# Kernel optimization log

Measured on AMD Instinct MI355X. Metric: run time of the kernel, lower is better.

The kernel has to match this reference:

```python
import jax, jax.numpy as jnp
import numpy as np

CODE_LEN = 1024
INFO_LEN = 512
BATCH = 2048
ITERS = 5
CLIP = 15.0
N_STAGES = 10  # log2(CODE_LEN)
DESIGN_SNR = 0.0


def _bhattacharyya_info_idx(N, K, snr_db):
    # standard polar code construction: Bhattacharyya parameter recursion
    z = np.array([np.exp(-10.0 ** (snr_db / 10.0))], dtype=np.float64)
    while z.size < N:
        z = np.concatenate([2.0 * z - z ** 2, z ** 2])
    return np.sort(np.argsort(z)[:K]).astype(np.int32)


def setup_inputs() -> dict:
    key = jax.random.key(0)
    rx = jax.random.normal(key, (BATCH, CODE_LEN), dtype=jnp.float32) * 4.0  # channel LLRs
    info_idx = jnp.asarray(_bhattacharyya_info_idx(CODE_LEN, INFO_LEN, DESIGN_SNR))
    return {"rx": rx, "info_idx": info_idx}


def _split(x, s):
    # pair elements (i, i + 2^s) within blocks of size 2^(s+1)
    B, N = x.shape
    st = 1 << s
    xr = x.reshape(B, N // (2 * st), 2, st)
    return xr[:, :, 0, :], xr[:, :, 1, :]


def _merge(u, l, s):
    B = u.shape[0]
    return jnp.stack([u, l], axis=2).reshape(B, -1)


def _f(a, b):
    # min-sum check-node update
    return jnp.sign(a) * jnp.sign(b) * jnp.minimum(jnp.abs(a), jnp.abs(b))


def _clip(x):
    return jnp.clip(x, -CLIP, CLIP)


def _iterate_right(right, left):
    # sweep info side (stage 0) -> channel side (stage n)
    cur = right[:, 0]
    stages = [cur]
    for s in range(N_STAGES):
        r_u, r_l = _split(cur, s)
        l_u, l_l = _split(left[:, s + 1], s)
        n_u = _clip(_f(r_u, l_l + r_l))
        n_l = _clip(_f(r_u, l_u) + r_l)
        cur = _merge(n_u, n_l, s)
        stages.append(cur)
    return jnp.stack(stages, axis=1)


def _iterate_left(right, left):
    # sweep channel side (stage n) -> info side (stage 0)
    cur = left[:, N_STAGES]
    stages = [cur]
    for s in range(N_STAGES - 1, -1, -1):
        l_u, l_l = _split(cur, s)
        r_u, r_l = _split(right[:, s], s)
        n_u = _clip(_f(l_u, l_l + r_l))
        n_l = _clip(_f(r_u, l_u) + l_l)
        cur = _merge(n_u, n_l, s)
        stages.append(cur)
    return jnp.stack(stages[::-1], axis=1)


def reference(rx, info_idx):
    B = rx.shape[0]
    mask = jnp.zeros((CODE_LEN,), rx.dtype).at[info_idx].set(1.0)
    # frozen positions carry +clip LLR, info positions 0 (crc=[], so total_info_bits == info mask)
    right = jnp.zeros((B, N_STAGES + 1, CODE_LEN), rx.dtype).at[:, 0].set((1.0 - mask) * CLIP)
    left = jnp.zeros_like(right).at[:, N_STAGES].set(rx)
    u_list = []
    for _ in range(ITERS):  # filter_in_iterations_eval=False -> all rows active every iteration
        right = _iterate_right(right, left)
        left = _iterate_left(right, left)
        u = left[:, 0] + right[:, 0]
        u_list.append(jnp.take(u, info_idx, axis=1))
    u_list.append(u_list[-1])  # u_list[-1] scatter reduces to last iterate when all rows active
    return jnp.stack(u_list)  # [ITERS+1, B, INFO_LEN]
```

## Files before the change

kernel.cpp:

```cpp
#include <hip/hip_runtime.h>

constexpr int CODE_LEN = 1024;
constexpr int INFO_LEN = 512;
constexpr int BATCH    = 2048;
constexpr int ITERS    = 5;
#define CLIPV 15.0f

__device__ __forceinline__ float fop(float a, float b) {
    unsigned x; float m, r;
    asm("v_xor_b32 %0, %1, %2" : "=v"(x) : "v"(a), "v"(b));
    asm("v_min_f32 %0, |%1|, |%2|" : "=v"(m) : "v"(a), "v"(b));
    asm("v_and_or_b32 %0, %1, %2, %3" : "=v"(r) : "v"(x), "s"(0x80000000u), "v"(m));
    return r;
}
__device__ __forceinline__ float clipf(float x) {
    return __builtin_amdgcn_fmed3f(x, -CLIPV, CLIPV);
}


#define RSTEP0(A, B) do { \
    float bu0=(B)[0], bl0=(B)[1], bu1=(B)[2], bl1=(B)[3]; \
    (B)[0]=fop((A)[0], bl0+(A)[1]); \
    (B)[1]=clipf(fop((A)[0], bu0)+(A)[1]); \
    (B)[2]=fop((A)[2], bl1+(A)[3]); \
    (B)[3]=clipf(fop((A)[2], bu1)+(A)[3]); } while(0)
#define RSTEP1(A, B) do { \
    float bu0=(B)[0], bl0=(B)[2], bu1=(B)[1], bl1=(B)[3]; \
    (B)[0]=fop((A)[0], bl0+(A)[2]); \
    (B)[2]=clipf(fop((A)[0], bu0)+(A)[2]); \
    (B)[1]=fop((A)[1], bl1+(A)[3]); \
    (B)[3]=clipf(fop((A)[1], bu1)+(A)[3]); } while(0)
#define LSTEP0(A, B) do { \
    float au0=(A)[0], al0=(A)[1], au1=(A)[2], al1=(A)[3]; \
    (A)[0]=fop((B)[0], (B)[1]+al0); \
    (A)[1]=clipf(fop(au0, (B)[0])+(B)[1]); \
    (A)[2]=fop((B)[2], (B)[3]+al1); \
    (A)[3]=clipf(fop(au1, (B)[2])+(B)[3]); } while(0)
#define LSTEP1(A, B) do { \
    float au0=(A)[0], al0=(A)[2], au1=(A)[1], al1=(A)[3]; \
    (A)[0]=fop((B)[0], (B)[2]+al0); \
    (A)[2]=clipf(fop(au0, (B)[0])+(B)[2]); \
    (A)[1]=fop((B)[1], (B)[3]+al1); \
    (A)[3]=clipf(fop(au1, (B)[1])+(B)[3]); } while(0)
#define LSTEP1C(A, B) do { \
    float au0=(A)[0], al0=(A)[2], au1=(A)[1], al1=(A)[3]; \
    (A)[0]=clipf(fop((B)[0], (B)[2]+al0)); \
    (A)[2]=clipf(fop(au0, (B)[0])+(B)[2]); \
    (A)[1]=clipf(fop((B)[1], (B)[3]+al1)); \
    (A)[3]=clipf(fop(au1, (B)[1])+(B)[3]); } while(0)
#define RSTEP0Z(A, B) do { \
    (B)[0]=fop((A)[0], (A)[1]); (B)[1]=(A)[1]; \
    (B)[2]=fop((A)[2], (A)[3]); (B)[3]=(A)[3]; } while(0)
#define RSTEP1Z(A, B) do { \
    (B)[0]=fop((A)[0], (A)[2]); (B)[2]=(A)[2]; \
    (B)[1]=fop((A)[1], (A)[3]); (B)[3]=(A)[3]; } while(0)

#define XBAR() do { \
    asm volatile("s_waitcnt lgkmcnt(0)" ::: "memory"); \
    __builtin_amdgcn_s_barrier(); \
    __builtin_amdgcn_sched_barrier(0); } while(0)

#define CONV_W(arr, WBASE, RBASE) do { \
    *(float4*)&WB[WBASE] = make_float4((arr)[0], (arr)[1], (arr)[2], (arr)[3]); \
    const float* rp_ = &WB[RBASE]; \
    float c0_ = rp_[0], c1_ = rp_[64], c2_ = rp_[128], c3_ = rp_[192]; \
    (arr)[0]=c0_; (arr)[1]=c1_; (arr)[2]=c2_; (arr)[3]=c3_; } while(0)

#define CONV_X(arr, XBUF) do { \
    float T0_ = mb0 ? (arr)[1] : (arr)[0]; \
    float T1_ = mb0 ? (arr)[0] : (arr)[1]; \
    float T2_ = mb0 ? (arr)[3] : (arr)[2]; \
    float T3_ = mb0 ? (arr)[2] : (arr)[3]; \
    float U0_ = mb1 ? T2_ : T0_; \
    float U1_ = mb1 ? T3_ : T1_; \
    float U2_ = mb1 ? T0_ : T2_; \
    float U3_ = mb1 ? T1_ : T3_; \
    *(float4*)&(XBUF)[wX] = make_float4(U0_, U1_, U2_, U3_); \
    XBAR(); \
    const float* xp_ = &(XBUF)[rX]; \
    float c0_ = xp_[0], c1_ = xp_[256], c2_ = xp_[512], c3_ = xp_[768]; \
    (arr)[0]=c0_; (arr)[1]=c1_; (arr)[2]=c2_; (arr)[3]=c3_; } while(0)

__global__ __launch_bounds__(256, 4) void polar_bp_r10(const float* __restrict__ rx,
                                                       const int* __restrict__ info,
                                                       float* __restrict__ out) {
    __shared__ int   RK[CODE_LEN];
    __shared__ float WB[CODE_LEN];
    __shared__ float XB0[CODE_LEN];
    __shared__ float XB1[CODE_LEN];

    const int t = threadIdx.x;
    const int b = blockIdx.x;

    *(int4*)&RK[t * 4] = make_int4(-1, -1, -1, -1);
    __syncthreads();
#pragma unroll
    for (int k = 0; k < 2; ++k) {
        int kk = t + 256 * k;
        int p  = info[kk];
        int fl = (p & 3) | (((p >> 6) & 3) << 2) | (((p >> 4) & 3) << 4)
               | (((p >> 2) & 3) << 6) | (((p >> 8) & 3) << 8);
        RK[fl] = kk;
    }
    __syncthreads();

    const int l6 = t & 63;
    const int w  = t >> 6;
    const int wbase = w * 256;
    const int wW4 = wbase + 4 * l6;
    const int rW4 = wbase + 4 * (l6 & 15) + ((l6 >> 4) & 3);
    const int wW2 = wbase + 4 * ((l6 & 3) | (((l6 >> 4) & 3) << 2) | (((l6 >> 2) & 3) << 4));
    const int rW2 = wbase + 4 * ((l6 & 3) | (((l6 >> 4) & 3) << 2)) + ((l6 >> 2) & 3);
    const int wW0 = wbase + 4 * (((l6 >> 2) & 15) | ((l6 & 3) << 4));
    const int rW0 = wbase + 4 * ((l6 >> 2) & 15) + (l6 & 3);
    const int  mX  = (l6 >> 3) & 3;
    const bool mb0 = (l6 & 8)  != 0;
    const bool mb1 = (l6 & 16) != 0;
    const int  wX  = 4 * l6 + 256 * w;
    const int  rX  = 4 * l6 + (w ^ mX);

    const int4 rkv = *(const int4*)&RK[t * 4];
    float fr[4];
    fr[0] = rkv.x < 0 ? CLIPV : 0.f;  fr[1] = rkv.y < 0 ? CLIPV : 0.f;
    fr[2] = rkv.z < 0 ? CLIPV : 0.f;  fr[3] = rkv.w < 0 ? CLIPV : 0.f;

    float S[10][4];
    {
        const float* rxb = rx + (size_t)b * CODE_LEN
                         + ((t >> 6) & 3) * 64 + (t & 3) * 16
                         + ((t >> 2) & 3) * 4 + ((t >> 4) & 3);
        S[9][0] = rxb[0];   S[9][1] = rxb[256];
        S[9][2] = rxb[512]; S[9][3] = rxb[768];
    }

    RSTEP0Z(fr, S[0]);
    RSTEP1Z(S[0], S[1]);
    CONV_W(S[1], wW4, rW4);
    RSTEP0Z(S[1], S[2]);
    RSTEP1Z(S[2], S[3]);
    CONV_W(S[3], wW2, rW2);
    RSTEP0Z(S[3], S[4]);
    RSTEP1Z(S[4], S[5]);
    CONV_W(S[5], wW0, rW0);
    RSTEP0Z(S[5], S[6]);
    RSTEP1Z(S[6], S[7]);
    CONV_X(S[7], XB0);
    RSTEP0Z(S[7], S[8]);

    float v0, v1, v2, v3;
    float* ob = out + (size_t)b * INFO_LEN;
    const size_t obstride = (size_t)BATCH * INFO_LEN;

#pragma unroll 1
    for (int it = 0; it < ITERS; ++it) {
        LSTEP1C(S[8], S[9]);
        LSTEP0(S[7], S[8]);
        CONV_X(S[7], XB1);
        LSTEP1(S[6], S[7]);
        LSTEP0(S[5], S[6]);
        CONV_W(S[5], wW0, rW0);
        LSTEP1(S[4], S[5]);
        LSTEP0(S[3], S[4]);
        CONV_W(S[3], wW2, rW2);
        LSTEP1(S[2], S[3]);
        LSTEP0(S[1], S[2]);
        CONV_W(S[1], wW4, rW4);
        LSTEP1(S[0], S[1]);
        v0 = fop(S[0][0], S[0][1] + fr[1]);
        v1 = clipf(fop(fr[0], S[0][0]) + S[0][1]);
        v2 = fop(S[0][2], S[0][3] + fr[3]);
        v3 = clipf(fop(fr[2], S[0][2]) + S[0][3]);
        if (rkv.x >= 0) ob[rkv.x] = v0;
        if (rkv.y >= 0) ob[rkv.y] = v1;
        if (rkv.z >= 0) ob[rkv.z] = v2;
        if (rkv.w >= 0) ob[rkv.w] = v3;
        ob += obstride;
        if (it != ITERS - 1) {
            RSTEP0(fr, S[0]);
            RSTEP1(S[0], S[1]);
            CONV_W(S[1], wW4, rW4);
            RSTEP0(S[1], S[2]);
            RSTEP1(S[2], S[3]);
            CONV_W(S[3], wW2, rW2);
            RSTEP0(S[3], S[4]);
            RSTEP1(S[4], S[5]);
            CONV_W(S[5], wW0, rW0);
            RSTEP0(S[5], S[6]);
            RSTEP1(S[6], S[7]);
            CONV_X(S[7], XB0);
            RSTEP0(S[7], S[8]);
        }
    }
    if (rkv.x >= 0) ob[rkv.x] = v0;
    if (rkv.y >= 0) ob[rkv.y] = v1;
    if (rkv.z >= 0) ob[rkv.z] = v2;
    if (rkv.w >= 0) ob[rkv.w] = v3;
}

extern "C" void kernel_launch(void* const* d_in, const int* in_sizes, int n_in,
                              void* d_out, int out_size, void* d_ws, size_t ws_size,
                              hipStream_t stream) {
    const float* rx   = (const float*)d_in[0];
    const int*   info = (const int*)d_in[1];
    float*       outp = (float*)d_out;
    polar_bp_r10<<<dim3(BATCH), dim3(256), 0, stream>>>(rx, info, outp);
}
```

Baseline: 32.71 us.

## Decode two codewords per block to amortize barriers and raise ILP

Each block now processes two batch rows, interleaving their stage updates so the two independent dependency chains can overlap. The cross-wave exchanges for both rows share a single barrier, and the grid is halved. This targets barrier and latency stalls per codeword. In exchange it doubles register state per thread (launch bounds lowered to 2 blocks per SM), uses more shared memory, and gives fewer blocks, all of which may reduce occupancy.

```diff
diff --git a/kernel.cpp b/kernel.cpp
--- a/kernel.cpp
+++ b/kernel.cpp
@@ -60,13 +60,13 @@
     __builtin_amdgcn_s_barrier(); \
     __builtin_amdgcn_sched_barrier(0); } while(0)
 
-#define CONV_W(arr, WBASE, RBASE) do { \
-    *(float4*)&WB[WBASE] = make_float4((arr)[0], (arr)[1], (arr)[2], (arr)[3]); \
-    const float* rp_ = &WB[RBASE]; \
+#define CONV_W(arr, WBp, WB_, RB_) do { \
+    *(float4*)&(WBp)[WB_] = make_float4((arr)[0], (arr)[1], (arr)[2], (arr)[3]); \
+    const float* rp_ = &(WBp)[RB_]; \
     float c0_ = rp_[0], c1_ = rp_[64], c2_ = rp_[128], c3_ = rp_[192]; \
     (arr)[0]=c0_; (arr)[1]=c1_; (arr)[2]=c2_; (arr)[3]=c3_; } while(0)
 
-#define CONV_X(arr, XBUF) do { \
+#define XPERM(arr, U0_, U1_, U2_, U3_) \
     float T0_ = mb0 ? (arr)[1] : (arr)[0]; \
     float T1_ = mb0 ? (arr)[0] : (arr)[1]; \
     float T2_ = mb0 ? (arr)[3] : (arr)[2]; \
@@ -74,20 +74,29 @@
     float U0_ = mb1 ? T2_ : T0_; \
     float U1_ = mb1 ? T3_ : T1_; \
     float U2_ = mb1 ? T0_ : T2_; \
-    float U3_ = mb1 ? T1_ : T3_; \
-    *(float4*)&(XBUF)[wX] = make_float4(U0_, U1_, U2_, U3_); \
+    float U3_ = mb1 ? T1_ : T3_;
+
+#define CONV_X2(arrA, arrB, XG) do { \
+    { XPERM(arrA, a0_, a1_, a2_, a3_) \
+      *(float4*)&(XG)[wX] = make_float4(a0_, a1_, a2_, a3_); } \
+    { XPERM(arrB, b0_, b1_, b2_, b3_) \
+      *(float4*)&(XG)[wX + 1024] = make_float4(b0_, b1_, b2_, b3_); } \
     XBAR(); \
-    const float* xp_ = &(XBUF)[rX]; \
-    float c0_ = xp_[0], c1_ = xp_[256], c2_ = xp_[512], c3_ = xp_[768]; \
-    (arr)[0]=c0_; (arr)[1]=c1_; (arr)[2]=c2_; (arr)[3]=c3_; } while(0)
-
-__global__ __launch_bounds__(256, 4) void polar_bp_r10(const float* __restrict__ rx,
+    { const float* xp_ = &(XG)[rX]; \
+      float c0_ = xp_[0], c1_ = xp_[256], c2_ = xp_[512], c3_ = xp_[768]; \
+      (arrA)[0]=c0_; (arrA)[1]=c1_; (arrA)[2]=c2_; (arrA)[3]=c3_; } \
+    { const float* xp_ = &(XG)[rX + 1024]; \
+      float c0_ = xp_[0], c1_ = xp_[256], c2_ = xp_[512], c3_ = xp_[768]; \
+      (arrB)[0]=c0_; (arrB)[1]=c1_; (arrB)[2]=c2_; (arrB)[3]=c3_; } } while(0)
+
+__global__ __launch_bounds__(256, 2) void polar_bp_r11(const float* __restrict__ rx,
                                                        const int* __restrict__ info,
                                                        float* __restrict__ out) {
     __shared__ int   RK[CODE_LEN];
-    __shared__ float WB[CODE_LEN];
-    __shared__ float XB0[CODE_LEN];
-    __shared__ float XB1[CODE_LEN];
+    __shared__ float WBA[CODE_LEN];
+    __shared__ float WBB[CODE_LEN];
+    __shared__ float XG0[2 * CODE_LEN];
+    __shared__ float XG1[2 * CODE_LEN];
 
     const int t = threadIdx.x;
     const int b = blockIdx.x;
@@ -119,82 +128,97 @@
     const int  wX  = 4 * l6 + 256 * w;
     const int  rX  = 4 * l6 + (w ^ mX);
 
-    const int4 rkv = *(const int4*)&RK[t * 4];
     float fr[4];
-    fr[0] = rkv.x < 0 ? CLIPV : 0.f;  fr[1] = rkv.y < 0 ? CLIPV : 0.f;
-    fr[2] = rkv.z < 0 ? CLIPV : 0.f;  fr[3] = rkv.w < 0 ? CLIPV : 0.f;
-
-    float S[10][4];
     {
-        const float* rxb = rx + (size_t)b * CODE_LEN
-                         + ((t >> 6) & 3) * 64 + (t & 3) * 16
-                         + ((t >> 2) & 3) * 4 + ((t >> 4) & 3);
-        S[9][0] = rxb[0];   S[9][1] = rxb[256];
-        S[9][2] = rxb[512]; S[9][3] = rxb[768];
-    }
-
-    RSTEP0Z(fr, S[0]);
-    RSTEP1Z(S[0], S[1]);
-    CONV_W(S[1], wW4, rW4);
-    RSTEP0Z(S[1], S[2]);
-    RSTEP1Z(S[2], S[3]);
-    CONV_W(S[3], wW2, rW2);
-    RSTEP0Z(S[3], S[4]);
-    RSTEP1Z(S[4], S[5]);
-    CONV_W(S[5], wW0, rW0);
-    RSTEP0Z(S[5], S[6]);
-    RSTEP1Z(S[6], S[7]);
-    CONV_X(S[7], XB0);
-    RSTEP0Z(S[7], S[8]);
-
-    float v0, v1, v2, v3;
-    float* ob = out + (size_t)b * INFO_LEN;
+        int4 rkv = *(const int4*)&RK[t * 4];
+        fr[0] = rkv.x < 0 ? CLIPV : 0.f;  fr[1] = rkv.y < 0 ? CLIPV : 0.f;
+        fr[2] = rkv.z < 0 ? CLIPV : 0.f;  fr[3] = rkv.w < 0 ? CLIPV : 0.f;
+    }
+
+    float SA[10][4], SB[10][4];
+    {
+        const int idx = ((t >> 6) & 3) * 64 + (t & 3) * 16
+                      + ((t >> 2) & 3) * 4 + ((t >> 4) & 3);
+        const float* rxa = rx + (size_t)(2 * b) * CODE_LEN + idx;
+        const float* rxb = rxa + CODE_LEN;
+        SA[9][0] = rxa[0];   SA[9][1] = rxa[256];
+        SA[9][2] = rxa[512]; SA[9][3] = rxa[768];
+        SB[9][0] = rxb[0];   SB[9][1] = rxb[256];
+        SB[9][2] = rxb[512]; SB[9][3] = rxb[768];
+    }
+
+    RSTEP0Z(fr, SA[0]);        RSTEP0Z(fr, SB[0]);
+    RSTEP1Z(SA[0], SA[1]);     RSTEP1Z(SB[0], SB[1]);
+    CONV_W(SA[1], WBA, wW4, rW4);  CONV_W(SB[1], WBB, wW4, rW4);
+    RSTEP0Z(SA[1], SA[2]);     RSTEP0Z(SB[1], SB[2]);
+    RSTEP1Z(SA[2], SA[3]);     RSTEP1Z(SB[2], SB[3]);
+    CONV_W(SA[3], WBA, wW2, rW2);  CONV_W(SB[3], WBB, wW2, rW2);
+    RSTEP0Z(SA[3], SA[4]);     RSTEP0Z(SB[3], SB[4]);
+    RSTEP1Z(SA[4], SA[5]);     RSTEP1Z(SB[4], SB[5]);
+    CONV_W(SA[5], WBA, wW0, rW0);  CONV_W(SB[5], WBB, wW0, rW0);
+    RSTEP0Z(SA[5], SA[6]);     RSTEP0Z(SB[5], SB[6]);
+    RSTEP1Z(SA[6], SA[7]);     RSTEP1Z(SB[6], SB[7]);
+    CONV_X2(SA[7], SB[7], XG0);
+    RSTEP0Z(SA[7], SA[8]);     RSTEP0Z(SB[7], SB[8]);
+
+    float vA0, vA1, vA2, vA3, vB0, vB1, vB2, vB3;
+    float* ob = out + (size_t)(2 * b) * INFO_LEN;
     const size_t obstride = (size_t)BATCH * INFO_LEN;
 
 #pragma unroll 1
     for (int it = 0; it < ITERS; ++it) {
-        LSTEP1C(S[8], S[9]);
-        LSTEP0(S[7], S[8]);
-        CONV_X(S[7], XB1);
-        LSTEP1(S[6], S[7]);
-        LSTEP0(S[5], S[6]);
-        CONV_W(S[5], wW0, rW0);
-        LSTEP1(S[4], S[5]);
-        LSTEP0(S[3], S[4]);
-        CONV_W(S[3], wW2, rW2);
-        LSTEP1(S[2], S[3]);
-        LSTEP0(S[1], S[2]);
-        CONV_W(S[1], wW4, rW4);
-        LSTEP1(S[0], S[1]);
-        v0 = fop(S[0][0], S[0][1] + fr[1]);
-        v1 = clipf(fop(fr[0], S[0][0]) + S[0][1]);
-        v2 = fop(S[0][2], S[0][3] + fr[3]);
-        v3 = clipf(fop(fr[2], S[0][2]) + S[0][3]);
-        if (rkv.x >= 0) ob[rkv.x] = v0;
-        if (rkv.y >= 0) ob[rkv.y] = v1;
-        if (rkv.z >= 0) ob[rkv.z] = v2;
-        if (rkv.w >= 0) ob[rkv.w] = v3;
+        LSTEP1C(SA[8], SA[9]);     LSTEP1C(SB[8], SB[9]);
+        LSTEP0(SA[7], SA[8]);      LSTEP0(SB[7], SB[8]);
+        CONV_X2(SA[7], SB[7], XG1);
+        LSTEP1(SA[6], SA[7]);      LSTEP1(SB[6], SB[7]);
+        LSTEP0(SA[5], SA[6]);      LSTEP0(SB[5], SB[6]);
+        CONV_W(SA[5], WBA, wW0, rW0);  CONV_W(SB[5], WBB, wW0, rW0);
+        LSTEP1(SA[4], SA[5]);      LSTEP1(SB[4], SB[5]);
+        LSTEP0(SA[3], SA[4]);      LSTEP0(SB[3], SB[4]);
+        CONV_W(SA[3], WBA, wW2, rW2);  CONV_W(SB[3], WBB, wW2, rW2);
+        LSTEP1(SA[2], SA[3]);      LSTEP1(SB[2], SB[3]);
+        LSTEP0(SA[1], SA[2]);      LSTEP0(SB[1], SB[2]);
+        CONV_W(SA[1], WBA, wW4, rW4);  CONV_W(SB[1], WBB, wW4, rW4);
+        LSTEP1(SA[0], SA[1]);      LSTEP1(SB[0], SB[1]);
+        vA0 = fop(SA[0][0], SA[0][1] + fr[1]);
+        vA1 = clipf(fop(fr[0], SA[0][0]) + SA[0][1]);
+        vA2 = fop(SA[0][2], SA[0][3] + fr[3]);
+        vA3 = clipf(fop(fr[2], SA[0][2]) + SA[0][3]);
+        vB0 = fop(SB[0][0], SB[0][1] + fr[1]);
+        vB1 = clipf(fop(fr[0], SB[0][0]) + SB[0][1]);
+        vB2 = fop(SB[0][2], SB[0][3] + fr[3]);
+        vB3 = clipf(fop(fr[2], SB[0][2]) + SB[0][3]);
+        {
+            int4 rkv = *(const int4*)&RK[t * 4];
+            if (rkv.x >= 0) { ob[rkv.x] = vA0; ob[rkv.x + INFO_LEN] = vB0; }
+            if (rkv.y >= 0) { ob[rkv.y] = vA1; ob[rkv.y + INFO_LEN] = vB1; }
+            if (rkv.z >= 0) { ob[rkv.z] = vA2; ob[rkv.z + INFO_LEN] = vB2; }
+            if (rkv.w >= 0) { ob[rkv.w] = vA3; ob[rkv.w + INFO_LEN] = vB3; }
+        }
         ob += obstride;
         if (it != ITERS - 1) {
-            RSTEP0(fr, S[0]);
-            RSTEP1(S[0], S[1]);
-            CONV_W(S[1], wW4, rW4);
-            RSTEP0(S[1], S[2]);
-            RSTEP1(S[2], S[3]);
-            CONV_W(S[3], wW2, rW2);
-            RSTEP0(S[3], S[4]);
-            RSTEP1(S[4], S[5]);
-            CONV_W(S[5], wW0, rW0);
-            RSTEP0(S[5], S[6]);
-            RSTEP1(S[6], S[7]);
-            CONV_X(S[7], XB0);
-            RSTEP0(S[7], S[8]);
+            RSTEP0(fr, SA[0]);         RSTEP0(fr, SB[0]);
+            RSTEP1(SA[0], SA[1]);      RSTEP1(SB[0], SB[1]);
+            CONV_W(SA[1], WBA, wW4, rW4);  CONV_W(SB[1], WBB, wW4, rW4);
+            RSTEP0(SA[1], SA[2]);      RSTEP0(SB[1], SB[2]);
+            RSTEP1(SA[2], SA[3]);      RSTEP1(SB[2], SB[3]);
+            CONV_W(SA[3], WBA, wW2, rW2);  CONV_W(SB[3], WBB, wW2, rW2);
+            RSTEP0(SA[3], SA[4]);      RSTEP0(SB[3], SB[4]);
+            RSTEP1(SA[4], SA[5]);      RSTEP1(SB[4], SB[5]);
+            CONV_W(SA[5], WBA, wW0, rW0);  CONV_W(SB[5], WBB, wW0, rW0);
+            RSTEP0(SA[5], SA[6]);      RSTEP0(SB[5], SB[6]);
+            RSTEP1(SA[6], SA[7]);      RSTEP1(SB[6], SB[7]);
+            CONV_X2(SA[7], SB[7], XG0);
+            RSTEP0(SA[7], SA[8]);      RSTEP0(SB[7], SB[8]);
         }
     }
-    if (rkv.x >= 0) ob[rkv.x] = v0;
-    if (rkv.y >= 0) ob[rkv.y] = v1;
-    if (rkv.z >= 0) ob[rkv.z] = v2;
-    if (rkv.w >= 0) ob[rkv.w] = v3;
+    {
+        int4 rkv = *(const int4*)&RK[t * 4];
+        if (rkv.x >= 0) { ob[rkv.x] = vA0; ob[rkv.x + INFO_LEN] = vB0; }
+        if (rkv.y >= 0) { ob[rkv.y] = vA1; ob[rkv.y + INFO_LEN] = vB1; }
+        if (rkv.z >= 0) { ob[rkv.z] = vA2; ob[rkv.z + INFO_LEN] = vB2; }
+        if (rkv.w >= 0) { ob[rkv.w] = vA3; ob[rkv.w + INFO_LEN] = vB3; }
+    }
 }
 
 extern "C" void kernel_launch(void* const* d_in, const int* in_sizes, int n_in,
@@ -203,5 +227,5 @@
     const float* rx   = (const float*)d_in[0];
     const int*   info = (const int*)d_in[1];
     float*       outp = (float*)d_out;
-    polar_bp_r10<<<dim3(BATCH), dim3(256), 0, stream>>>(rx, info, outp);
-}
+    polar_bp_r11<<<dim3(BATCH / 2), dim3(256), 0, stream>>>(rx, info, outp);
+}
```

New measurement: 34.39 us. 1.05x slower.

## Replace intra-wave LDS transposes with DPP and permlane swaps

Applied to the files above, without the earlier changes.

The three within-wavefront data transposes, which used to go through a shared-memory write/read buffer, are now done with cross-lane DPP moves and permlane16/permlane32 swap instructions. This removes LDS traffic and its latency from the per-stage exchange path and frees the WB shared buffer. The cost is extra VALU select and mov work, and a fallback to ds_swizzle when permlane16_swap is unavailable. The min-sum helper is also rewritten with intrinsics instead of inline asm, which gives the compiler room to schedule it.

```diff
diff --git a/kernel.cpp b/kernel.cpp
--- a/kernel.cpp
+++ b/kernel.cpp
@@ -7,16 +7,55 @@
 #define CLIPV 15.0f
 
 __device__ __forceinline__ float fop(float a, float b) {
-    unsigned x; float m, r;
-    asm("v_xor_b32 %0, %1, %2" : "=v"(x) : "v"(a), "v"(b));
-    asm("v_min_f32 %0, |%1|, |%2|" : "=v"(m) : "v"(a), "v"(b));
-    asm("v_and_or_b32 %0, %1, %2, %3" : "=v"(r) : "v"(x), "s"(0x80000000u), "v"(m));
-    return r;
+    unsigned s = __float_as_uint(a) ^ __float_as_uint(b);
+    float m = fminf(fabsf(a), fabsf(b));
+    return copysignf(m, __uint_as_float(s));
 }
 __device__ __forceinline__ float clipf(float x) {
     return __builtin_amdgcn_fmed3f(x, -CLIPV, CLIPV);
 }
 
+
+template<int CTRL>
+__device__ __forceinline__ float dppmv(float x) {
+    return __int_as_float(__builtin_amdgcn_mov_dpp(__float_as_int(x), CTRL, 0xf, 0xf, true));
+}
+__device__ __forceinline__ float dppx1(float x) { return dppmv<0xB1>(x); }
+__device__ __forceinline__ float dppx2(float x) { return dppmv<0x4E>(x); }
+__device__ __forceinline__ float dppx4(float x) { return dppmv<0x1B>(dppmv<0x141>(x)); }
+__device__ __forceinline__ float dppx8(float x) { return dppmv<0x141>(dppmv<0x140>(x)); }
+
+typedef unsigned u32x2 __attribute__((ext_vector_type(2)));
+
+#define BSW(P, Q, DPPFN, BIT) do { \
+    float pa_ = DPPFN(P), pb_ = DPPFN(Q); \
+    bool c_ = (l6 & (BIT)) != 0; \
+    P = c_ ? pb_ : P;  Q = c_ ? Q : pa_; } while(0)
+
+#if __has_builtin(__builtin_amdgcn_permlane16_swap)
+#define PL16(P, Q) do { \
+    u32x2 r_ = __builtin_amdgcn_permlane16_swap(__float_as_uint(P), __float_as_uint(Q), false, false); \
+    P = __uint_as_float(r_[0]); Q = __uint_as_float(r_[1]); } while(0)
+#else
+__device__ __forceinline__ float swzx16(float x) {
+    return __int_as_float(__builtin_amdgcn_ds_swizzle(__float_as_int(x), 0x401F));
+}
+#define PL16(P, Q) BSW(P, Q, swzx16, 16)
+#endif
+
+#define PL32(P, Q) do { \
+    u32x2 r_ = __builtin_amdgcn_permlane32_swap(__float_as_uint(P), __float_as_uint(Q), false, false); \
+    P = __uint_as_float(r_[0]); Q = __uint_as_float(r_[1]); } while(0)
+
+#define CONV_R4(S) do { \
+    PL16((S)[0], (S)[1]); PL16((S)[2], (S)[3]); \
+    PL32((S)[0], (S)[2]); PL32((S)[1], (S)[3]); } while(0)
+#define CONV_R2(S) do { \
+    BSW((S)[0], (S)[1], dppx4, 4);  BSW((S)[2], (S)[3], dppx4, 4); \
+    BSW((S)[0], (S)[2], dppx8, 8);  BSW((S)[1], (S)[3], dppx8, 8); } while(0)
+#define CONV_R0(S) do { \
+    BSW((S)[0], (S)[1], dppx1, 1);  BSW((S)[2], (S)[3], dppx1, 1); \
+    BSW((S)[0], (S)[2], dppx2, 2);  BSW((S)[1], (S)[3], dppx2, 2); } while(0)
 
 #define RSTEP0(A, B) do { \
     float bu0=(B)[0], bl0=(B)[1], bu1=(B)[2], bl1=(B)[3]; \
@@ -60,12 +99,6 @@
     __builtin_amdgcn_s_barrier(); \
     __builtin_amdgcn_sched_barrier(0); } while(0)
 
-#define CONV_W(arr, WBASE, RBASE) do { \
-    *(float4*)&WB[WBASE] = make_float4((arr)[0], (arr)[1], (arr)[2], (arr)[3]); \
-    const float* rp_ = &WB[RBASE]; \
-    float c0_ = rp_[0], c1_ = rp_[64], c2_ = rp_[128], c3_ = rp_[192]; \
-    (arr)[0]=c0_; (arr)[1]=c1_; (arr)[2]=c2_; (arr)[3]=c3_; } while(0)
-
 #define CONV_X(arr, XBUF) do { \
     float T0_ = mb0 ? (arr)[1] : (arr)[0]; \
     float T1_ = mb0 ? (arr)[0] : (arr)[1]; \
@@ -81,11 +114,10 @@
     float c0_ = xp_[0], c1_ = xp_[256], c2_ = xp_[512], c3_ = xp_[768]; \
     (arr)[0]=c0_; (arr)[1]=c1_; (arr)[2]=c2_; (arr)[3]=c3_; } while(0)
 
-__global__ __launch_bounds__(256, 4) void polar_bp_r10(const float* __restrict__ rx,
+__global__ __launch_bounds__(256, 4) void polar_bp_r13(const float* __restrict__ rx,
                                                        const int* __restrict__ info,
                                                        float* __restrict__ out) {
     __shared__ int   RK[CODE_LEN];
-    __shared__ float WB[CODE_LEN];
     __shared__ float XB0[CODE_LEN];
     __shared__ float XB1[CODE_LEN];
 
@@ -106,13 +138,6 @@
 
     const int l6 = t & 63;
     const int w  = t >> 6;
-    const int wbase = w * 256;
-    const int wW4 = wbase + 4 * l6;
-    const int rW4 = wbase + 4 * (l6 & 15) + ((l6 >> 4) & 3);
-    const int wW2 = wbase + 4 * ((l6 & 3) | (((l6 >> 4) & 3) << 2) | (((l6 >> 2) & 3) << 4));
-    const int rW2 = wbase + 4 * ((l6 & 3) | (((l6 >> 4) & 3) << 2)) + ((l6 >> 2) & 3);
-    const int wW0 = wbase + 4 * (((l6 >> 2) & 15) | ((l6 & 3) << 4));
-    const int rW0 = wbase + 4 * ((l6 >> 2) & 15) + (l6 & 3);
     const int  mX  = (l6 >> 3) & 3;
     const bool mb0 = (l6 & 8)  != 0;
     const bool mb1 = (l6 & 16) != 0;
@@ -135,13 +160,13 @@
 
     RSTEP0Z(fr, S[0]);
     RSTEP1Z(S[0], S[1]);
-    CONV_W(S[1], wW4, rW4);
+    CONV_R4(S[1]);
     RSTEP0Z(S[1], S[2]);
     RSTEP1Z(S[2], S[3]);
-    CONV_W(S[3], wW2, rW2);
+    CONV_R2(S[3]);
     RSTEP0Z(S[3], S[4]);
     RSTEP1Z(S[4], S[5]);
-    CONV_W(S[5], wW0, rW0);
+    CONV_R0(S[5]);
     RSTEP0Z(S[5], S[6]);
     RSTEP1Z(S[6], S[7]);
     CONV_X(S[7], XB0);
@@ -158,13 +183,13 @@
         CONV_X(S[7], XB1);
         LSTEP1(S[6], S[7]);
         LSTEP0(S[5], S[6]);
-        CONV_W(S[5], wW0, rW0);
+        CONV_R0(S[5]);
         LSTEP1(S[4], S[5]);
         LSTEP0(S[3], S[4]);
-        CONV_W(S[3], wW2, rW2);
+        CONV_R2(S[3]);
         LSTEP1(S[2], S[3]);
         LSTEP0(S[1], S[2]);
-        CONV_W(S[1], wW4, rW4);
+        CONV_R4(S[1]);
         LSTEP1(S[0], S[1]);
         v0 = fop(S[0][0], S[0][1] + fr[1]);
         v1 = clipf(fop(fr[0], S[0][0]) + S[0][1]);
@@ -178,13 +203,13 @@
         if (it != ITERS - 1) {
             RSTEP0(fr, S[0]);
             RSTEP1(S[0], S[1]);
-            CONV_W(S[1], wW4, rW4);
+            CONV_R4(S[1]);
             RSTEP0(S[1], S[2]);
             RSTEP1(S[2], S[3]);
-            CONV_W(S[3], wW2, rW2);
+            CONV_R2(S[3]);
             RSTEP0(S[3], S[4]);
             RSTEP1(S[4], S[5]);
-            CONV_W(S[5], wW0, rW0);
+            CONV_R0(S[5]);
             RSTEP0(S[5], S[6]);
             RSTEP1(S[6], S[7]);
             CONV_X(S[7], XB0);
@@ -203,5 +228,5 @@
     const float* rx   = (const float*)d_in[0];
     const int*   info = (const int*)d_in[1];
     float*       outp = (float*)d_out;
-    polar_bp_r10<<<dim3(BATCH), dim3(256), 0, stream>>>(rx, info, outp);
-}
+    polar_bp_r13<<<dim3(BATCH), dim3(256), 0, stream>>>(rx, info, outp);
+}
```

Measured after the change: 40.37 us. 1.23x slower.
